# Optimization experiments

Measured on AMD Instinct MI355X. Metric: run time of the kernel, lower is better.

Reference implementation:

```python
import jax, jax.numpy as jnp
import numpy as np

BN_EPS = 1e-5
N_OUT, D_OUT = 64, 128


def setup_inputs() -> dict:
    key = jax.random.key(0)
    k1, k2, k3, k4 = jax.random.split(key, 4)
    B, N_in, D_in, K = 512, 64, 128, 4
    x = jax.random.normal(k1, (B, N_in, D_in), dtype=jnp.float32)
    # block-sparse weights: one (D_in x D_out) block per (output-row, active-input-row) pair
    W = jax.random.normal(k2, (N_OUT, K, D_in, D_OUT), dtype=jnp.float32) * (1.0 / np.sqrt(K * D_in))
    bias = jax.random.normal(k3, (N_OUT, D_OUT), dtype=jnp.float32) * 0.02
    gamma = jnp.ones((N_OUT * D_OUT,), dtype=jnp.float32)
    beta = jnp.zeros((N_OUT * D_OUT,), dtype=jnp.float32)
    idx = jax.random.randint(k4, (N_OUT, K), 0, N_in, dtype=jnp.int32)
    return {"x": x, "W": W, "bias": bias, "gamma": gamma, "beta": beta, "idx": idx}


def reference(x, W, bias, gamma, beta, idx):
    B = x.shape[0]
    # structured-sparse linear: gather active input rows, per-block matmul
    xg = x[:, idx, :]                                   # [B, N_out, K, D_in]
    y = jnp.einsum('bokd,okde->boe', xg, W) + bias      # [B, N_out, D_out]
    # BatchNorm1d (training-mode batch statistics) on flattened features
    yf = y.reshape(B, -1)                               # [B, N_out*D_out]
    mean = jnp.mean(yf, axis=0)
    var = jnp.mean(jnp.square(yf - mean), axis=0)       # biased variance, as in torch BN
    yn = (yf - mean) * jax.lax.rsqrt(var + BN_EPS) * gamma + beta
    # Swish: z * sigmoid(z)
    out = yn * jax.nn.sigmoid(yn)
    return out.reshape(B, N_OUT, D_OUT)
```

## Files before the change

### kernel.cpp

```cpp
#include <hip/hip_runtime.h>


typedef __attribute__((ext_vector_type(8))) __bf16 bf16x8;
typedef __attribute__((ext_vector_type(4))) float  f32x4;

#define FEAT 8192
#define XROW 8192
#define LDB  40

#define PIPE_BARRIER() do { \
    __builtin_amdgcn_sched_barrier(0); \
    asm volatile("s_waitcnt lgkmcnt(0)" ::: "memory"); \
    __builtin_amdgcn_s_barrier(); \
    __builtin_amdgcn_sched_barrier(0); \
} while (0)

__global__ __launch_bounds__(1024, 4)
void fused_encoder(const float* __restrict__ x, const float* __restrict__ W,
                   const float* __restrict__ bias, const float* __restrict__ gamma,
                   const float* __restrict__ beta, const int* __restrict__ idxp,
                   float* __restrict__ out)
{
    __shared__ alignas(16) __bf16 Blds[2][32 * LDB];
    __shared__ float Sred[16][32];
    __shared__ float Qred[16][32];
    __shared__ float sscale[32];
    __shared__ float sshift[32];

    const int bid = blockIdx.x;
    const int o   = ((bid >> 5) << 3) | (bid & 7);
    const int es  = (bid >> 3) & 3;
    const int e0  = es * 32;

    const int tid  = threadIdx.x;
    const int wave = tid >> 6;
    const int lane = tid & 63;
    const int lam  = lane & 15;
    const int quad = lane >> 4;

    int rsel[4];
#pragma unroll
    for (int k = 0; k < 4; ++k) rsel[k] = idxp[o * 4 + k];

    const f32x4 zero4 = {0.f, 0.f, 0.f, 0.f};
    f32x4 acc[2][2];
#pragma unroll
    for (int mi = 0; mi < 2; ++mi)
#pragma unroll
        for (int ni = 0; ni < 2; ++ni) acc[mi][ni] = zero4;

    const float* xrow0 = x + (wave * 32 + lam)      * XROW;
    const float* xrow1 = x + (wave * 32 + 16 + lam) * XROW;

    const int e_b = tid & 31;
    const int d_b = tid >> 5;

    f32x4 sa0[4], sa1[4];
    float sb0, sb1;

    auto loadA = [&](f32x4 (&SA)[4], const int kkc) {
        const int r  = rsel[kkc >> 2];
        const int dd = (kkc & 3) * 32 + quad * 8;
        const float* p0 = xrow0 + r * 128 + dd;
        const float* p1 = xrow1 + r * 128 + dd;
        SA[0] = *(const f32x4*)(p0);
        SA[1] = *(const f32x4*)(p0 + 4);
        SA[2] = *(const f32x4*)(p1);
        SA[3] = *(const f32x4*)(p1 + 4);
    };
    auto loadB = [&](float& SB, const int kkc) {
        const int kidx = kkc >> 2;
        const int d0   = (kkc & 3) * 32;
        SB = W[(((o * 4 + kidx) * 128) + d0 + d_b) * 128 + e0 + e_b];
    };
    auto storeB = [&](const float SB, const int buf) {
        Blds[buf][e_b * LDB + d_b] = (__bf16)SB;
    };
    auto cvtA = [&](const f32x4 (&SA)[4], bf16x8 (&af)[2]) {
#pragma unroll
        for (int j = 0; j < 4; ++j) {
            af[0][j]     = (__bf16)SA[0][j];
            af[0][j + 4] = (__bf16)SA[1][j];
            af[1][j]     = (__bf16)SA[2][j];
            af[1][j + 4] = (__bf16)SA[3][j];
        }
    };
    auto mma = [&](const bf16x8 (&af)[2], const int buf) {
        bf16x8 bfr[2];
#pragma unroll
        for (int ni = 0; ni < 2; ++ni)
            bfr[ni] = *(const bf16x8*)&Blds[buf][(ni * 16 + lam) * LDB + quad * 8];
#pragma unroll
        for (int mi = 0; mi < 2; ++mi)
#pragma unroll
            for (int ni = 0; ni < 2; ++ni)
                acc[mi][ni] = __builtin_amdgcn_mfma_f32_16x16x32_bf16(
                    af[mi], bfr[ni], acc[mi][ni], 0, 0, 0);
    };

    loadA(sa0, 0); loadB(sb0, 0);
    loadA(sa1, 1); loadB(sb1, 1);
    storeB(sb0, 0);
    PIPE_BARRIER();

#pragma unroll
    for (int kk = 0; kk < 16; ++kk) {
        bf16x8 af[2];
        if ((kk & 1) == 0) {
            cvtA(sa0, af);
            if (kk + 2 < 16) { loadA(sa0, kk + 2); loadB(sb0, kk + 2); }
        } else {
            cvtA(sa1, af);
            if (kk + 2 < 16) { loadA(sa1, kk + 2); loadB(sb1, kk + 2); }
        }
        __builtin_amdgcn_sched_barrier(0);
        mma(af, kk & 1);
        if (kk + 1 < 16) {
            if ((kk & 1) == 0) storeB(sb1, 1);
            else               storeB(sb0, 0);
            PIPE_BARRIER();
        }
    }

    float bvals[2];
#pragma unroll
    for (int ni = 0; ni < 2; ++ni)
        bvals[ni] = bias[o * 128 + e0 + ni * 16 + lam];
#pragma unroll
    for (int mi = 0; mi < 2; ++mi)
#pragma unroll
        for (int ni = 0; ni < 2; ++ni)
#pragma unroll
            for (int rr = 0; rr < 4; ++rr) acc[mi][ni][rr] += bvals[ni];

#pragma unroll
    for (int ni = 0; ni < 2; ++ni) {
        float s = 0.f, q = 0.f;
#pragma unroll
        for (int mi = 0; mi < 2; ++mi)
#pragma unroll
            for (int rr = 0; rr < 4; ++rr) {
                const float v = acc[mi][ni][rr];
                s += v; q += v * v;
            }
        s += __shfl_xor(s, 16); s += __shfl_xor(s, 32);
        q += __shfl_xor(q, 16); q += __shfl_xor(q, 32);
        if (quad == 0) {
            Sred[wave][ni * 16 + lam] = s;
            Qred[wave][ni * 16 + lam] = q;
        }
    }
    __syncthreads();

    if (tid < 32) {
        float s = 0.f, q = 0.f;
#pragma unroll
        for (int w = 0; w < 16; ++w) {
            s += Sred[w][tid];
            q += Qred[w][tid];
        }
        const float mean = s * (1.0f / 512.0f);
        const float var  = q * (1.0f / 512.0f) - mean * mean;
        const float rstd = rsqrtf(var + 1e-5f);
        const float sc   = rstd * gamma[o * 128 + e0 + tid];
        sscale[tid] = sc;
        sshift[tid] = beta[o * 128 + e0 + tid] - mean * sc;
    }
    __syncthreads();

#pragma unroll
    for (int mi = 0; mi < 2; ++mi) {
        const int rowb = wave * 32 + mi * 16 + quad * 4;
#pragma unroll
        for (int ni = 0; ni < 2; ++ni) {
            const int col = ni * 16 + lam;
            const float sc = sscale[col];
            const float sh = sshift[col];
#pragma unroll
            for (int rr = 0; rr < 4; ++rr) {
                const float xn = acc[mi][ni][rr] * sc + sh;
                const float sg = 1.0f / (1.0f + __expf(-xn));
                out[(rowb + rr) * FEAT + o * 128 + e0 + col] = xn * sg;
            }
        }
    }
}

extern "C" void kernel_launch(void* const* d_in, const int* in_sizes, int n_in,
                              void* d_out, int out_size, void* d_ws, size_t ws_size,
                              hipStream_t stream)
{
    const float* x     = (const float*)d_in[0];
    const float* W     = (const float*)d_in[1];
    const float* bias  = (const float*)d_in[2];
    const float* gamma = (const float*)d_in[3];
    const float* beta  = (const float*)d_in[4];
    const int*   idx   = (const int*)d_in[5];
    float* out = (float*)d_out;

    fused_encoder<<<dim3(256), dim3(1024), 0, stream>>>(
        x, W, bias, gamma, beta, idx, out);
}
```

Before: 114.4 us.

## Preload full W panel into LDS once, drop per-step barriers in K loop

Instead of streaming each 32-deep W slice into a double-buffered LDS tile with a barrier on every K step, the block loads its entire 512x32 weight panel (converted to bf16) into LDS once before the loop, behind a single __syncthreads. The main loop then only prefetches x rows and does the MFMAs, removing fifteen block-wide barriers and the interleaved W loads. The cost is a larger LDS footprint (about 33 KB) and an up-front W load that no longer overlaps with the first MFMAs.

```diff
diff --git a/kernel.cpp b/kernel.cpp
--- a/kernel.cpp
+++ b/kernel.cpp
@@ -6,14 +6,7 @@
 
 #define FEAT 8192
 #define XROW 8192
-#define LDB  40
-
-#define PIPE_BARRIER() do { \
-    __builtin_amdgcn_sched_barrier(0); \
-    asm volatile("s_waitcnt lgkmcnt(0)" ::: "memory"); \
-    __builtin_amdgcn_s_barrier(); \
-    __builtin_amdgcn_sched_barrier(0); \
-} while (0)
+#define LDSB 520
 
 __global__ __launch_bounds__(1024, 4)
 void fused_encoder(const float* __restrict__ x, const float* __restrict__ W,
@@ -21,7 +14,7 @@
                    const float* __restrict__ beta, const int* __restrict__ idxp,
                    float* __restrict__ out)
 {
-    __shared__ alignas(16) __bf16 Blds[2][32 * LDB];
+    __shared__ __bf16 Bpan[32 * LDSB];
     __shared__ float Sred[16][32];
     __shared__ float Qred[16][32];
     __shared__ float sscale[32];
@@ -42,6 +35,25 @@
 #pragma unroll
     for (int k = 0; k < 4; ++k) rsel[k] = idxp[o * 4 + k];
 
+    {
+        const int e  = tid & 31;
+        const int k0 = (tid >> 5) * 16;
+        float v[16];
+#pragma unroll
+        for (int j = 0; j < 16; ++j) {
+            const int k = k0 + j;
+            v[j] = W[(((o * 4 + (k >> 7)) * 128) + (k & 127)) * 128 + e0 + e];
+        }
+        bf16x8 w0, w1;
+#pragma unroll
+        for (int j = 0; j < 8; ++j) {
+            w0[j] = (__bf16)v[j];
+            w1[j] = (__bf16)v[8 + j];
+        }
+        *(bf16x8*)&Bpan[e * LDSB + k0]     = w0;
+        *(bf16x8*)&Bpan[e * LDSB + k0 + 8] = w1;
+    }
+
     const f32x4 zero4 = {0.f, 0.f, 0.f, 0.f};
     f32x4 acc[2][2];
 #pragma unroll
@@ -52,11 +64,7 @@
     const float* xrow0 = x + (wave * 32 + lam)      * XROW;
     const float* xrow1 = x + (wave * 32 + 16 + lam) * XROW;
 
-    const int e_b = tid & 31;
-    const int d_b = tid >> 5;
-
     f32x4 sa0[4], sa1[4];
-    float sb0, sb1;
 
     auto loadA = [&](f32x4 (&SA)[4], const int kkc) {
         const int r  = rsel[kkc >> 2];
@@ -68,14 +76,6 @@
         SA[2] = *(const f32x4*)(p1);
         SA[3] = *(const f32x4*)(p1 + 4);
     };
-    auto loadB = [&](float& SB, const int kkc) {
-        const int kidx = kkc >> 2;
-        const int d0   = (kkc & 3) * 32;
-        SB = W[(((o * 4 + kidx) * 128) + d0 + d_b) * 128 + e0 + e_b];
-    };
-    auto storeB = [&](const float SB, const int buf) {
-        Blds[buf][e_b * LDB + d_b] = (__bf16)SB;
-    };
     auto cvtA = [&](const f32x4 (&SA)[4], bf16x8 (&af)[2]) {
 #pragma unroll
         for (int j = 0; j < 4; ++j) {
@@ -85,41 +85,27 @@
             af[1][j + 4] = (__bf16)SA[3][j];
         }
     };
-    auto mma = [&](const bf16x8 (&af)[2], const int buf) {
-        bf16x8 bfr[2];
-#pragma unroll
-        for (int ni = 0; ni < 2; ++ni)
-            bfr[ni] = *(const bf16x8*)&Blds[buf][(ni * 16 + lam) * LDB + quad * 8];
-#pragma unroll
-        for (int mi = 0; mi < 2; ++mi)
-#pragma unroll
-            for (int ni = 0; ni < 2; ++ni)
-                acc[mi][ni] = __builtin_amdgcn_mfma_f32_16x16x32_bf16(
-                    af[mi], bfr[ni], acc[mi][ni], 0, 0, 0);
-    };
 
-    loadA(sa0, 0); loadB(sb0, 0);
-    loadA(sa1, 1); loadB(sb1, 1);
-    storeB(sb0, 0);
-    PIPE_BARRIER();
+    loadA(sa0, 0);
+    loadA(sa1, 1);
+    __syncthreads();
 
 #pragma unroll
     for (int kk = 0; kk < 16; ++kk) {
         bf16x8 af[2];
         if ((kk & 1) == 0) {
             cvtA(sa0, af);
-            if (kk + 2 < 16) { loadA(sa0, kk + 2); loadB(sb0, kk + 2); }
+            if (kk + 2 < 16) loadA(sa0, kk + 2);
         } else {
             cvtA(sa1, af);
-            if (kk + 2 < 16) { loadA(sa1, kk + 2); loadB(sb1, kk + 2); }
+            if (kk + 2 < 16) loadA(sa1, kk + 2);
         }
-        __builtin_amdgcn_sched_barrier(0);
-        mma(af, kk & 1);
-        if (kk + 1 < 16) {
-            if ((kk & 1) == 0) storeB(sb1, 1);
-            else               storeB(sb0, 0);
-            PIPE_BARRIER();
-        }
+        const bf16x8 b0 = *(const bf16x8*)&Bpan[lam        * LDSB + kk * 32 + quad * 8];
+        const bf16x8 b1 = *(const bf16x8*)&Bpan[(16 + lam) * LDSB + kk * 32 + quad * 8];
+        acc[0][0] = __builtin_amdgcn_mfma_f32_16x16x32_bf16(af[0], b0, acc[0][0], 0, 0, 0);
+        acc[0][1] = __builtin_amdgcn_mfma_f32_16x16x32_bf16(af[0], b1, acc[0][1], 0, 0, 0);
+        acc[1][0] = __builtin_amdgcn_mfma_f32_16x16x32_bf16(af[1], b0, acc[1][0], 0, 0, 0);
+        acc[1][1] = __builtin_amdgcn_mfma_f32_16x16x32_bf16(af[1], b1, acc[1][1], 0, 0, 0);
     }
 
     float bvals[2];
```

Measured after the change: 115.6 us. Within noise of the previous version (+1.0%).
